# Kernel optimization log

Hardware: AMD Instinct MI355X
Metric: run time of the kernel (lower is better)

## Reference

```python
import jax, jax.numpy as jnp
import numpy as np

B, T, N = 32, 64, 36
VD, H, S = 2048, 512, 300


def setup_inputs() -> dict:
    key = jax.random.key(0)
    ks = jax.random.split(key, 24)
    sc = 0.02
    d = {
        "visual": jax.random.normal(ks[0], (B, T, VD), jnp.float32),
        "objects": jax.random.normal(ks[1], (B, N, H), jnp.float32),
        # linear_layer
        "lin_W": jax.random.normal(ks[2], (H, VD), jnp.float32) * sc,
        "lin_b": jnp.zeros((H,), jnp.float32),
        # W, U projections
        "W_W": jax.random.normal(ks[3], (H, H), jnp.float32) * sc,
        "W_b": jnp.zeros((H,), jnp.float32),
        "U_W": jax.random.normal(ks[4], (H, H), jnp.float32) * sc,
        "U_b": jnp.zeros((H,), jnp.float32),
        # additive attention bias (torch.ones init)
        "b_attn": jnp.ones((H,), jnp.float32),
        # scoring vector w: Linear(H, 1)
        "w_W": jax.random.normal(ks[5], (1, H), jnp.float32) * sc,
        "w_b": jnp.zeros((1,), jnp.float32),
        # BiLSTM: input 2H, hidden H//2 per direction; gate order i,f,g,o
        "Wih_f": jax.random.normal(ks[6], (4 * (H // 2), 2 * H), jnp.float32) * sc,
        "Whh_f": jax.random.normal(ks[7], (4 * (H // 2), H // 2), jnp.float32) * sc,
        "bih_f": jnp.zeros((4 * (H // 2),), jnp.float32),
        "bhh_f": jnp.zeros((4 * (H // 2),), jnp.float32),
        "Wih_b": jax.random.normal(ks[8], (4 * (H // 2), 2 * H), jnp.float32) * sc,
        "Whh_b": jax.random.normal(ks[9], (4 * (H // 2), H // 2), jnp.float32) * sc,
        "bih_b": jnp.zeros((4 * (H // 2),), jnp.float32),
        "bhh_b": jnp.zeros((4 * (H // 2),), jnp.float32),
        # fc_layer
        "fc_W": jax.random.normal(ks[10], (S, H), jnp.float32) * sc,
        "fc_b": jnp.zeros((S,), jnp.float32),
    }
    return d


def _lstm(x, Wih, Whh, b):
    """Unidirectional LSTM over time. x: [B, T, D] -> [B, T, Hc]."""
    bsz = x.shape[0]
    Hc = Whh.shape[1]

    def step(carry, xt):
        h, c = carry
        g = xt @ Wih.T + h @ Whh.T + b          # [B, 4Hc]
        i, f, gg, o = jnp.split(g, 4, axis=-1)  # torch gate order i,f,g,o
        c = jax.nn.sigmoid(f) * c + jax.nn.sigmoid(i) * jnp.tanh(gg)
        h = jax.nn.sigmoid(o) * jnp.tanh(c)
        return (h, c), h

    h0 = jnp.zeros((bsz, Hc), x.dtype)
    _, hs = jax.lax.scan(step, (h0, h0), jnp.swapaxes(x, 0, 1))
    return jnp.swapaxes(hs, 0, 1)


def reference(visual, objects, lin_W, lin_b, W_W, W_b, U_W, U_b, b_attn,
              w_W, w_b, Wih_f, Whh_f, bih_f, bhh_f, Wih_b, Whh_b, bih_b,
              bhh_b, fc_W, fc_b):
    f3d = visual @ lin_W.T + lin_b                 # [B, T, H]
    Wf = f3d @ W_W.T + W_b                         # [B, T, H]
    Uo = objects @ U_W.T + U_b                     # [B, N, H]
    # broadcast additive attention: [B, T, N, H]
    attn_feat = Wf[:, :, None, :] + Uo[:, None, :, :] + b_attn
    scores = jnp.tanh(attn_feat) @ w_W.T + w_b     # [B, T, N, 1]
    attn_w = jax.nn.softmax(scores, axis=-2)       # softmax over objects N
    attn_obj = (attn_w * attn_feat).sum(axis=-2)   # [B, T, H]
    feats = jnp.concatenate([f3d, attn_obj], axis=-1)  # [B, T, 2H]
    out_f = _lstm(feats, Wih_f, Whh_f, bih_f + bhh_f)
    out_b = _lstm(feats[:, ::-1, :], Wih_b, Whh_b, bih_b + bhh_b)[:, ::-1, :]
    output = jnp.concatenate([out_f, out_b], axis=-1)  # [B, T, H]
    action = jnp.max(output, axis=1)                   # [B, H]
    action_semantics = action @ fc_W.T + fc_b          # [B, S]
    return output, action_semantics
```

## Files before the change

### kernel.cpp

```cpp
#include <hip/hip_runtime.h>
#include <hip/hip_bf16.h>
#include <type_traits>


typedef __hip_bfloat16 bf16;
typedef __attribute__((ext_vector_type(8))) short s8v;
typedef __attribute__((ext_vector_type(4))) float f4v;

__device__ inline f4v mfma16(s8v a, s8v b, f4v c) {
    return __builtin_amdgcn_mfma_f32_16x16x32_bf16(a, b, c, 0, 0, 0);
}

__device__ inline float sigf(float x) {
    return __builtin_amdgcn_rcpf(1.f + __expf(-x));
}
__device__ inline float tanh_(float x) {
    return 1.f - 2.f * __builtin_amdgcn_rcpf(1.f + __expf(2.f * x));
}

struct CvtJobs {
    const float* src[9];
    bf16*        dst[9];
    int          start[10];
};

__global__ __launch_bounds__(256) void cvt_kernel(CvtJobs jobs) {
    int blk = blockIdx.x;
    int j = 0;
#pragma unroll
    for (int i = 1; i < 9; ++i) if (blk >= jobs.start[i]) j = i;
    int off = (blk - jobs.start[j]) * 1024 + threadIdx.x * 4;
    float4 v = *(const float4*)(jobs.src[j] + off);
    union { bf16 h[4]; uint2 u; } p;
    p.h[0] = __float2bfloat16(v.x);
    p.h[1] = __float2bfloat16(v.y);
    p.h[2] = __float2bfloat16(v.z);
    p.h[3] = __float2bfloat16(v.w);
    *(uint2*)(jobs.dst[j] + off) = p.u;
}

template <typename CT>
__global__ __launch_bounds__(256) void gemm_bt(
    const bf16* __restrict__ A, int lda,
    const bf16* __restrict__ W,
    const float* __restrict__ b1, const float* __restrict__ b2,
    CT* __restrict__ C, int ldc,
    int K, int tiles_n, int permuteTB)
{
    int w    = blockIdx.x * 4 + (threadIdx.x >> 6);
    int lane = threadIdx.x & 63;
    int mt = w / tiles_n, nt = w % tiles_n;
    int lo = lane & 15, hi = lane >> 4;

    const bf16* a0 = A + (size_t)(mt * 32 + lo) * lda + hi * 8;
    const bf16* a1 = a0 + (size_t)16 * lda;
    const bf16* w0 = W + (size_t)(nt * 32 + lo) * K + hi * 8;
    const bf16* w1 = w0 + (size_t)16 * K;

    f4v acc00 = {0.f,0.f,0.f,0.f}, acc01 = {0.f,0.f,0.f,0.f};
    f4v acc10 = {0.f,0.f,0.f,0.f}, acc11 = {0.f,0.f,0.f,0.f};

    for (int k = 0; k < K; k += 32) {
        s8v af0 = *(const s8v*)(a0 + k);
        s8v af1 = *(const s8v*)(a1 + k);
        s8v wf0 = *(const s8v*)(w0 + k);
        s8v wf1 = *(const s8v*)(w1 + k);
        acc00 = mfma16(af0, wf0, acc00);
        acc01 = mfma16(af0, wf1, acc01);
        acc10 = mfma16(af1, wf0, acc10);
        acc11 = mfma16(af1, wf1, acc11);
    }

    int c0 = nt * 32 + lo, c1 = c0 + 16;
    float bv0 = b1 ? b1[c0] : 0.f;
    float bv1 = b1 ? b1[c1] : 0.f;
    if (b2) { bv0 += b2[c0]; bv1 += b2[c1]; }

    int r0 = mt * 32 + hi * 4;
#pragma unroll
    for (int i = 0; i < 4; ++i) {
        int ra = r0 + i;
        int rb = ra + 16;
        int rra = permuteTB ? ((ra & 63) * 32 + (ra >> 6)) : ra;
        int rrb = permuteTB ? ((rb & 63) * 32 + (rb >> 6)) : rb;
        float v;
        v = acc00[i] + bv0;
        if constexpr (std::is_same<CT, float>::value) C[(size_t)rra * ldc + c0] = v;
        else C[(size_t)rra * ldc + c0] = __float2bfloat16(v);
        v = acc01[i] + bv1;
        if constexpr (std::is_same<CT, float>::value) C[(size_t)rra * ldc + c1] = v;
        else C[(size_t)rra * ldc + c1] = __float2bfloat16(v);
        v = acc10[i] + bv0;
        if constexpr (std::is_same<CT, float>::value) C[(size_t)rrb * ldc + c0] = v;
        else C[(size_t)rrb * ldc + c0] = __float2bfloat16(v);
        v = acc11[i] + bv1;
        if constexpr (std::is_same<CT, float>::value) C[(size_t)rrb * ldc + c1] = v;
        else C[(size_t)rrb * ldc + c1] = __float2bfloat16(v);
    }
}

__global__ __launch_bounds__(256) void attn_kernel(
    const float* __restrict__ Wf,
    const float* __restrict__ Uo,
    const float* __restrict__ wW,
    const float* __restrict__ wB,
    bf16* __restrict__ feats)
{
    int bt = blockIdx.x, b = bt >> 6;
    int wv = threadIdx.x >> 6, lane = threadIdx.x & 63;
    __shared__ float s_aw[36];

    float wfr[8], wr[8];
    const float* wfrow = Wf + (size_t)bt * 512 + lane * 8;
#pragma unroll
    for (int i = 0; i < 8; ++i) {
        wfr[i] = wfrow[i];
        wr[i]  = wW[lane * 8 + i];
    }
    float wbv = wB[0];

    for (int n = wv; n < 36; n += 4) {
        const float* uo = Uo + ((size_t)b * 36 + n) * 512 + lane * 8;
        float s = 0.f;
#pragma unroll
        for (int i = 0; i < 8; ++i) s += wr[i] * tanh_(wfr[i] + uo[i]);
#pragma unroll
        for (int off = 32; off; off >>= 1) s += __shfl_xor(s, off);
        if (lane == 0) s_aw[n] = s + wbv;
    }
    __syncthreads();
    if (threadIdx.x == 0) {
        float mx = -1e30f;
#pragma unroll
        for (int n = 0; n < 36; ++n) mx = fmaxf(mx, s_aw[n]);
        float e[36], sum = 0.f;
#pragma unroll
        for (int n = 0; n < 36; ++n) { e[n] = __expf(s_aw[n] - mx); sum += e[n]; }
        float r = __builtin_amdgcn_rcpf(sum);
#pragma unroll
        for (int n = 0; n < 36; ++n) s_aw[n] = e[n] * r;
    }
    __syncthreads();

    int h0 = threadIdx.x * 2;
    const float* wf2 = Wf + (size_t)bt * 512 + h0;
    float a0 = wf2[0], a1 = wf2[1];
    for (int n = 0; n < 36; ++n) {
        float awn = s_aw[n];
        const float* uo = Uo + ((size_t)b * 36 + n) * 512 + h0;
        a0 += awn * uo[0];
        a1 += awn * uo[1];
    }
    feats[(size_t)bt * 1024 + 512 + h0]     = __float2bfloat16(a0);
    feats[(size_t)bt * 1024 + 512 + h0 + 1] = __float2bfloat16(a1);
}

__device__ inline void grid_bar(int* bar, int target) {
    __threadfence();
    __syncthreads();
    if (threadIdx.x == 0) {
        __hip_atomic_fetch_add(bar, 1, __ATOMIC_ACQ_REL, __HIP_MEMORY_SCOPE_AGENT);
        while (__hip_atomic_load(bar, __ATOMIC_ACQUIRE, __HIP_MEMORY_SCOPE_AGENT) < target) {
            __builtin_amdgcn_s_sleep(2);
        }
    }
    __syncthreads();
}

__global__ __launch_bounds__(256, 1) void lstm_kernel(
    const bf16* __restrict__ WhhF, const bf16* __restrict__ WhhB,
    const float* __restrict__ gatesF, const float* __restrict__ gatesB,
    bf16* __restrict__ hbuf,
    float* __restrict__ out,
    int* __restrict__ bar)
{
    int bi  = blockIdx.x;
    int dir = bi >> 2;
    int jb  = (bi & 3) * 64;
    int wv = threadIdx.x >> 6, lane = threadIdx.x & 63;
    int lo = lane & 15, hi = lane >> 4;

    const bf16*  Whh   = dir ? WhhB : WhhF;
    const float* gates = dir ? gatesB : gatesF;
    bf16* hb   = hbuf + (size_t)dir * 2 * 32 * 256;
    int* mybar = bar + dir * 16;
    int j0 = jb + wv * 16;

    s8v whhF[4][8];
#pragma unroll
    for (int g = 0; g < 4; ++g)
#pragma unroll
        for (int kt = 0; kt < 8; ++kt)
            whhF[g][kt] = *(const s8v*)(Whh + (size_t)(g * 256 + j0 + lo) * 256 + kt * 32 + hi * 8);

    for (int x = threadIdx.x; x < 2048; x += 256) {
        int b = x >> 6, j = jb + (x & 63);
        hb[b * 256 + j] = __float2bfloat16(0.f);
    }

    float cst[2][4] = {{0.f,0.f,0.f,0.f},{0.f,0.f,0.f,0.f}};
    int phase = 0;
    grid_bar(mybar, 4 * (++phase));

    for (int t = 0; t < 64; ++t) {
        const bf16* hr = hb + (t & 1) * (32 * 256);
        bf16*       hw = hb + ((t & 1) ^ 1) * (32 * 256);
        int tp = dir ? (63 - t) : t;
        const float* gin = gates + (size_t)tp * 32 * 1024;

        float gv[2][4][4];
#pragma unroll
        for (int m = 0; m < 2; ++m)
#pragma unroll
            for (int i = 0; i < 4; ++i) {
                int b = m * 16 + hi * 4 + i;
#pragma unroll
                for (int g = 0; g < 4; ++g)
                    gv[m][g][i] = gin[(size_t)b * 1024 + g * 256 + j0 + lo];
            }

        s8v aF[2][8];
#pragma unroll
        for (int m = 0; m < 2; ++m)
#pragma unroll
            for (int kt = 0; kt < 8; ++kt)
                aF[m][kt] = *(const s8v*)(hr + (m * 16 + lo) * 256 + kt * 32 + hi * 8);

        f4v acc[2][4];
#pragma unroll
        for (int m = 0; m < 2; ++m)
#pragma unroll
            for (int g = 0; g < 4; ++g) acc[m][g] = (f4v){0.f,0.f,0.f,0.f};
#pragma unroll
        for (int kt = 0; kt < 8; ++kt)
#pragma unroll
            for (int m = 0; m < 2; ++m)
#pragma unroll
                for (int g = 0; g < 4; ++g)
                    acc[m][g] = mfma16(aF[m][kt], whhF[g][kt], acc[m][g]);

#pragma unroll
        for (int m = 0; m < 2; ++m)
#pragma unroll
            for (int i = 0; i < 4; ++i) {
                float xi = acc[m][0][i] + gv[m][0][i];
                float xf = acc[m][1][i] + gv[m][1][i];
                float xg = acc[m][2][i] + gv[m][2][i];
                float xo = acc[m][3][i] + gv[m][3][i];
                float c = sigf(xf) * cst[m][i] + sigf(xi) * tanh_(xg);
                cst[m][i] = c;
                float h = sigf(xo) * tanh_(c);
                int b = m * 16 + hi * 4 + i, j = j0 + lo;
                hw[b * 256 + j] = __float2bfloat16(h);
                out[((size_t)b * 64 + tp) * 512 + dir * 256 + j] = h;
            }

        grid_bar(mybar, 4 * (++phase));
    }
}

__global__ __launch_bounds__(256) void final_kernel(
    const float* __restrict__ out,
    const float* __restrict__ fcW,
    const float* __restrict__ fcb,
    float* __restrict__ osem)
{
    int b = blockIdx.x, tid = threadIdx.x;
    __shared__ float act[512];
    for (int h = tid; h < 512; h += 256) {
        float m = -1e30f;
        const float* p = out + (size_t)b * 64 * 512 + h;
#pragma unroll 8
        for (int t = 0; t < 64; ++t) m = fmaxf(m, p[t * 512]);
        act[h] = m;
    }
    __syncthreads();
    int wv = tid >> 6, lane = tid & 63;
    for (int s = wv; s < 300; s += 4) {
        const float* wrow = fcW + (size_t)s * 512 + lane * 8;
        float a = 0.f;
#pragma unroll
        for (int i = 0; i < 8; ++i) a += act[lane * 8 + i] * wrow[i];
#pragma unroll
        for (int off = 32; off; off >>= 1) a += __shfl_xor(a, off);
        if (lane == 0) osem[b * 300 + s] = a + fcb[s];
    }
}

extern "C" void kernel_launch(void* const* d_in, const int* in_sizes, int n_in,
                              void* d_out, int out_size, void* d_ws, size_t ws_size,
                              hipStream_t stream)
{
    const float* visual  = (const float*)d_in[0];
    const float* objects = (const float*)d_in[1];
    const float* lin_W   = (const float*)d_in[2];
    const float* lin_b   = (const float*)d_in[3];
    const float* W_W     = (const float*)d_in[4];
    const float* W_b     = (const float*)d_in[5];
    const float* U_W     = (const float*)d_in[6];
    const float* U_b     = (const float*)d_in[7];
    const float* b_attn  = (const float*)d_in[8];
    const float* w_W     = (const float*)d_in[9];
    const float* w_b     = (const float*)d_in[10];
    const float* Wih_f   = (const float*)d_in[11];
    const float* Whh_f   = (const float*)d_in[12];
    const float* bih_f   = (const float*)d_in[13];
    const float* bhh_f   = (const float*)d_in[14];
    const float* Wih_b   = (const float*)d_in[15];
    const float* Whh_b   = (const float*)d_in[16];
    const float* bih_b   = (const float*)d_in[17];
    const float* bhh_b   = (const float*)d_in[18];
    const float* fc_W    = (const float*)d_in[19];
    const float* fc_b    = (const float*)d_in[20];

    char* ws = (char*)d_ws;
    size_t o = 0;
    bf16*  feats   = (bf16*)(ws + o);  o += (size_t)2048 * 1024 * 2;
    float* Wf      = (float*)(ws + o); o += (size_t)2048 * 512 * 4;
    float* Uo      = (float*)(ws + o); o += (size_t)1152 * 512 * 4;
    float* gatesF  = (float*)(ws + o); o += (size_t)2048 * 1024 * 4;
    float* gatesB  = (float*)(ws + o); o += (size_t)2048 * 1024 * 4;
    bf16*  hbuf    = (bf16*)(ws + o);  o += (size_t)2 * 2 * 32 * 256 * 2;
    int*   bar     = (int*)(ws + o);   o += 256;
    bf16*  visual_b  = (bf16*)(ws + o); o += (size_t)4194304 * 2;
    bf16*  objects_b = (bf16*)(ws + o); o += (size_t)589824 * 2;
    bf16*  lin_Wb    = (bf16*)(ws + o); o += (size_t)1048576 * 2;
    bf16*  W_Wb      = (bf16*)(ws + o); o += (size_t)262144 * 2;
    bf16*  U_Wb      = (bf16*)(ws + o); o += (size_t)262144 * 2;
    bf16*  Wih_fb    = (bf16*)(ws + o); o += (size_t)1048576 * 2;
    bf16*  Whh_fb    = (bf16*)(ws + o); o += (size_t)262144 * 2;
    bf16*  Wih_bb    = (bf16*)(ws + o); o += (size_t)1048576 * 2;
    bf16*  Whh_bb    = (bf16*)(ws + o); o += (size_t)262144 * 2;

    hipMemsetAsync(bar, 0, 256, stream);

    CvtJobs cj;
    const float* srcs[9] = {visual, objects, lin_W, W_W, U_W, Wih_f, Whh_f, Wih_b, Whh_b};
    bf16* dsts[9] = {visual_b, objects_b, lin_Wb, W_Wb, U_Wb, Wih_fb, Whh_fb, Wih_bb, Whh_bb};
    int ns[9] = {4194304, 589824, 1048576, 262144, 262144, 1048576, 262144, 1048576, 262144};
    int acc_b = 0;
    for (int i = 0; i < 9; ++i) {
        cj.src[i] = srcs[i];
        cj.dst[i] = dsts[i];
        cj.start[i] = acc_b;
        acc_b += ns[i] / 1024;
    }
    cj.start[9] = acc_b;

    dim3 blk(256);
    cvt_kernel<<<acc_b, blk, 0, stream>>>(cj);

    gemm_bt<bf16><<<256, blk, 0, stream>>>(visual_b, 2048, lin_Wb, lin_b, nullptr,
                                           feats, 1024, 2048, 16, 0);
    gemm_bt<float><<<144, blk, 0, stream>>>(objects_b, 512, U_Wb, U_b, b_attn,
                                            Uo, 512, 512, 16, 0);
    gemm_bt<float><<<256, blk, 0, stream>>>(feats, 1024, W_Wb, W_b, nullptr,
                                            Wf, 512, 512, 16, 0);
    attn_kernel<<<2048, blk, 0, stream>>>(Wf, Uo, w_W, w_b, feats);
    gemm_bt<float><<<512, blk, 0, stream>>>(feats, 1024, Wih_fb, bih_f, bhh_f,
                                            gatesF, 1024, 1024, 32, 1);
    gemm_bt<float><<<512, blk, 0, stream>>>(feats, 1024, Wih_bb, bih_b, bhh_b,
                                            gatesB, 1024, 1024, 32, 1);
    lstm_kernel<<<8, blk, 0, stream>>>(Whh_fb, Whh_bb, gatesF, gatesB, hbuf,
                                       (float*)d_out, bar);
    final_kernel<<<32, blk, 0, stream>>>((float*)d_out, fc_W, fc_b,
                                         (float*)d_out + 1048576);
}
```

Baseline: 620.1 us.

## Use relaxed agent-scope atomics for LSTM hidden-state exchange and barrier

Replaces the grid barrier's threadfence and acquire/release atomics with relaxed atomics and drops the sleep in the spin loop. The hidden state is now exchanged as packed bf16 pairs through per-word agent-scope atomic stores and loads, using a lane shuffle to pair neighbouring outputs. The aim is to cut per-timestep cross-block synchronisation latency in the 64-step recurrence. The cost is weaker memory ordering, which relies on atomic coherence to keep the hidden-state handoff correct, plus scalar 32-bit loads in place of 128-bit vector loads.

```diff
diff --git a/kernel.cpp b/kernel.cpp
--- a/kernel.cpp
+++ b/kernel.cpp
@@ -4,6 +4,7 @@
 
 
 typedef __hip_bfloat16 bf16;
+typedef unsigned int uint32;
 typedef __attribute__((ext_vector_type(8))) short s8v;
 typedef __attribute__((ext_vector_type(4))) float f4v;
 
@@ -156,13 +157,10 @@
 }
 
 __device__ inline void grid_bar(int* bar, int target) {
-    __threadfence();
     __syncthreads();
     if (threadIdx.x == 0) {
-        __hip_atomic_fetch_add(bar, 1, __ATOMIC_ACQ_REL, __HIP_MEMORY_SCOPE_AGENT);
-        while (__hip_atomic_load(bar, __ATOMIC_ACQUIRE, __HIP_MEMORY_SCOPE_AGENT) < target) {
-            __builtin_amdgcn_s_sleep(2);
-        }
+        __hip_atomic_fetch_add(bar, 1, __ATOMIC_RELAXED, __HIP_MEMORY_SCOPE_AGENT);
+        while (__hip_atomic_load(bar, __ATOMIC_RELAXED, __HIP_MEMORY_SCOPE_AGENT) < target) {}
     }
     __syncthreads();
 }
@@ -170,7 +168,7 @@
 __global__ __launch_bounds__(256, 1) void lstm_kernel(
     const bf16* __restrict__ WhhF, const bf16* __restrict__ WhhB,
     const float* __restrict__ gatesF, const float* __restrict__ gatesB,
-    bf16* __restrict__ hbuf,
+    uint32* __restrict__ hx,
     float* __restrict__ out,
     int* __restrict__ bar)
 {
@@ -182,7 +180,7 @@
 
     const bf16*  Whh   = dir ? WhhB : WhhF;
     const float* gates = dir ? gatesB : gatesF;
-    bf16* hb   = hbuf + (size_t)dir * 2 * 32 * 256;
+    uint32* hxd  = hx + (size_t)dir * 2 * 32 * 128;
     int* mybar = bar + dir * 16;
     int j0 = jb + wv * 16;
 
@@ -193,9 +191,9 @@
         for (int kt = 0; kt < 8; ++kt)
             whhF[g][kt] = *(const s8v*)(Whh + (size_t)(g * 256 + j0 + lo) * 256 + kt * 32 + hi * 8);
 
-    for (int x = threadIdx.x; x < 2048; x += 256) {
-        int b = x >> 6, j = jb + (x & 63);
-        hb[b * 256 + j] = __float2bfloat16(0.f);
+    for (int x = threadIdx.x; x < 1024; x += 256) {
+        int b = x >> 5, jw = (jb >> 1) + (x & 31);
+        __hip_atomic_store(&hxd[b * 128 + jw], 0u, __ATOMIC_RELAXED, __HIP_MEMORY_SCOPE_AGENT);
     }
 
     float cst[2][4] = {{0.f,0.f,0.f,0.f},{0.f,0.f,0.f,0.f}};
@@ -203,8 +201,8 @@
     grid_bar(mybar, 4 * (++phase));
 
     for (int t = 0; t < 64; ++t) {
-        const bf16* hr = hb + (t & 1) * (32 * 256);
-        bf16*       hw = hb + ((t & 1) ^ 1) * (32 * 256);
+        const uint32* hr = hxd + (t & 1) * (32 * 128);
+        uint32*       hw = hxd + ((t & 1) ^ 1) * (32 * 128);
         int tp = dir ? (63 - t) : t;
         const float* gin = gates + (size_t)tp * 32 * 1024;
 
@@ -223,8 +221,15 @@
 #pragma unroll
         for (int m = 0; m < 2; ++m)
 #pragma unroll
-            for (int kt = 0; kt < 8; ++kt)
-                aF[m][kt] = *(const s8v*)(hr + (m * 16 + lo) * 256 + kt * 32 + hi * 8);
+            for (int kt = 0; kt < 8; ++kt) {
+                union { uint32 u[4]; s8v v; } tt;
+                int base = (m * 16 + lo) * 128 + kt * 16 + hi * 4;
+#pragma unroll
+                for (int q = 0; q < 4; ++q)
+                    tt.u[q] = __hip_atomic_load(&hr[base + q], __ATOMIC_RELAXED,
+                                                __HIP_MEMORY_SCOPE_AGENT);
+                aF[m][kt] = tt.v;
+            }
 
         f4v acc[2][4];
 #pragma unroll
@@ -239,6 +244,7 @@
                 for (int g = 0; g < 4; ++g)
                     acc[m][g] = mfma16(aF[m][kt], whhF[g][kt], acc[m][g]);
 
+        float hv[2][4];
 #pragma unroll
         for (int m = 0; m < 2; ++m)
 #pragma unroll
@@ -250,9 +256,23 @@
                 float c = sigf(xf) * cst[m][i] + sigf(xi) * tanh_(xg);
                 cst[m][i] = c;
                 float h = sigf(xo) * tanh_(c);
-                int b = m * 16 + hi * 4 + i, j = j0 + lo;
-                hw[b * 256 + j] = __float2bfloat16(h);
-                out[((size_t)b * 64 + tp) * 512 + dir * 256 + j] = h;
+                hv[m][i] = h;
+                int b = m * 16 + hi * 4 + i;
+                out[((size_t)b * 64 + tp) * 512 + dir * 256 + j0 + lo] = h;
+            }
+
+#pragma unroll
+        for (int m = 0; m < 2; ++m)
+#pragma unroll
+            for (int i = 0; i < 4; ++i) {
+                float o2 = __shfl_xor(hv[m][i], 1);
+                if (!(lane & 1)) {
+                    uint32 p = (uint32)__bfloat16_as_ushort(__float2bfloat16(hv[m][i]))
+                             | ((uint32)__bfloat16_as_ushort(__float2bfloat16(o2)) << 16);
+                    int b = m * 16 + hi * 4 + i;
+                    __hip_atomic_store(&hw[b * 128 + ((j0 + lo) >> 1)], p,
+                                       __ATOMIC_RELAXED, __HIP_MEMORY_SCOPE_AGENT);
+                }
             }
 
         grid_bar(mybar, 4 * (++phase));
@@ -315,13 +335,13 @@
 
     char* ws = (char*)d_ws;
     size_t o = 0;
-    bf16*  feats   = (bf16*)(ws + o);  o += (size_t)2048 * 1024 * 2;
-    float* Wf      = (float*)(ws + o); o += (size_t)2048 * 512 * 4;
-    float* Uo      = (float*)(ws + o); o += (size_t)1152 * 512 * 4;
-    float* gatesF  = (float*)(ws + o); o += (size_t)2048 * 1024 * 4;
-    float* gatesB  = (float*)(ws + o); o += (size_t)2048 * 1024 * 4;
-    bf16*  hbuf    = (bf16*)(ws + o);  o += (size_t)2 * 2 * 32 * 256 * 2;
-    int*   bar     = (int*)(ws + o);   o += 256;
+    bf16*   feats   = (bf16*)(ws + o);   o += (size_t)2048 * 1024 * 2;
+    float*  Wf      = (float*)(ws + o);  o += (size_t)2048 * 512 * 4;
+    float*  Uo      = (float*)(ws + o);  o += (size_t)1152 * 512 * 4;
+    float*  gatesF  = (float*)(ws + o);  o += (size_t)2048 * 1024 * 4;
+    float*  gatesB  = (float*)(ws + o);  o += (size_t)2048 * 1024 * 4;
+    uint32* hx      = (uint32*)(ws + o); o += (size_t)2 * 2 * 32 * 128 * 4;
+    int*    bar     = (int*)(ws + o);    o += 256;
     bf16*  visual_b  = (bf16*)(ws + o); o += (size_t)4194304 * 2;
     bf16*  objects_b = (bf16*)(ws + o); o += (size_t)589824 * 2;
     bf16*  lin_Wb    = (bf16*)(ws + o); o += (size_t)1048576 * 2;
@@ -361,7 +381,7 @@
                                             gatesF, 1024, 1024, 32, 1);
     gemm_bt<float><<<512, blk, 0, stream>>>(feats, 1024, Wih_bb, bih_b, bhh_b,
                                             gatesB, 1024, 1024, 32, 1);
-    lstm_kernel<<<8, blk, 0, stream>>>(Whh_fb, Whh_bb, gatesF, gatesB, hbuf,
+    lstm_kernel<<<8, blk, 0, stream>>>(Whh_fb, Whh_bb, gatesF, gatesB, hx,
                                        (float*)d_out, bar);
     final_kernel<<<32, blk, 0, stream>>>((float*)d_out, fc_W, fc_b,
                                          (float*)d_out + 1048576);
```

Result: slower. 885.3 us (+42.8%).
